# Kernel tuning notes

Hardware: AMD Instinct MI355X
Metric: run time of the kernel (lower is better)

The kernel has to match this reference:

```python
import jax, jax.numpy as jnp
import numpy as np

T, B, C, HS, RD = 32, 32, 128, 512, 3  # timesteps, batch, state_channels, hidden_size, recurse_depth
HW = 7


def setup_inputs() -> dict:
    key = jax.random.key(0)
    ks = jax.random.split(key, 6)
    x = jax.random.normal(ks[0], (T * B, C, HW, HW), jnp.float32)
    hxs = jax.random.normal(ks[1], (B, 2 * C, HW, HW), jnp.float32)
    masks = jax.random.uniform(ks[2], (T * B,), jnp.float32)
    # ConvLSTMCell: conv over concat(x, h) [2C in] -> 4C gate channels, 3x3, bias
    Wconv = jax.random.normal(ks[3], (4 * C, 2 * C, 3, 3), jnp.float32) * 0.02
    bconv = jnp.zeros((4 * C,), jnp.float32)
    # flat_lin: Linear(C*7*7 -> hidden_size), torch layout [out, in]
    Wlin = jax.random.normal(ks[4], (HS, C * HW * HW), jnp.float32) * 0.02
    blin = jnp.zeros((HS,), jnp.float32)
    return {"x": x, "hxs": hxs, "masks": masks, "Wconv": Wconv, "bconv": bconv, "Wlin": Wlin, "blin": blin}


def reference(x, hxs, masks, Wconv, bconv, Wlin, blin):
    xs = x.reshape(T, B, C, HW, HW)
    ms = masks.reshape(T, B)
    h0, c0 = hxs[:, :C], hxs[:, C:]

    def conv_gates(inp):  # [B, 2C, 7, 7] -> [B, 4C, 7, 7]
        y = jax.lax.conv_general_dilated(
            inp, Wconv, window_strides=(1, 1), padding="SAME",
            dimension_numbers=("NCHW", "OIHW", "NCHW"))
        return y + bconv[None, :, None, None]

    def step(carry, inp):
        h, c = carry
        x_t, m_t = inp
        m = m_t[:, None, None, None]
        h = h * m
        c = c * m
        for _ in range(RD):  # recurse_depth inner unroll (sequential dependency)
            g = conv_gates(jnp.concatenate([x_t, h], axis=1))
            cc_i, cc_f, cc_o, cc_g = jnp.split(g, 4, axis=1)
            i = jax.nn.sigmoid(cc_i)
            f = jax.nn.sigmoid(cc_f)
            o = jax.nn.sigmoid(cc_o)
            gg = jnp.tanh(cc_g)
            c = f * c + i * gg
            h = o * jnp.tanh(c)
        out = jax.nn.relu(c.reshape(B, -1) @ Wlin.T + blin)  # flat_lin applied to c
        return (h, c), out

    (hT, cT), outs = jax.lax.scan(step, (h0, c0), (xs, ms))
    return outs.reshape(T * B, HS), jnp.concatenate([hT, cT], axis=1)
```

## Files before the change

kernel.cpp:

```cpp
#include <hip/hip_runtime.h>
#include <hip/hip_bf16.h>
#include <stdint.h>

#define T_  32
#define B_  32
#define C_  128
#define HS_ 512
#define HW_ 7
#define S_  49
#define CS_  (C_*S_)
#define ICS_ (2*C_*S_)
#define KH_  1152
#define KL_  6272
#define M_   1568
#define MR_  1600
#define N_   512

typedef __attribute__((ext_vector_type(8))) short short8;
typedef __attribute__((ext_vector_type(4))) float f32x4;
typedef __hip_bfloat16 bf16;

union bfbits { bf16 b; short s; };

__device__ __forceinline__ void gl16(const void* g, void* l) {
    __builtin_amdgcn_global_load_lds((const __attribute__((address_space(1))) void*)g,
                                     (__attribute__((address_space(3))) void*)l, 16, 0, 0);
}

__device__ __forceinline__ float sigm_f(float v) { return 1.0f / (1.0f + __expf(-v)); }
__device__ __forceinline__ float tanh_f(float v) { return 1.0f - 2.0f / (__expf(2.0f * v) + 1.0f); }

__global__ __launch_bounds__(256, 2) void k_fgemm(
    const bf16* __restrict__ xTt, const bf16* __restrict__ hT,
    bf16* __restrict__ hTN,
    const bf16* __restrict__ WxP, const bf16* __restrict__ WhP,
    const float* __restrict__ bconv,
    float* __restrict__ Gx, float* __restrict__ cbuf,
    const float* __restrict__ mask_c, const float* __restrict__ mask_a,
    bf16* __restrict__ chist_t, const bf16* __restrict__ zb, int mode0)
{
    __shared__ __align__(16) uint8_t smem[65536];
    bf16* sA = (bf16*)smem;
    bf16* sB = (bf16*)(smem + 32768);
    float (*gld)[68] = (float(*)[68])smem;

    const int tid = threadIdx.x, lane = tid & 63, w = tid >> 6;
    const int wr = w >> 1, wc = w & 1;
    const int m0 = blockIdx.x * 64, n0 = blockIdx.y * 64;

    const int kq = tid & 15, rr = tid >> 4;
    const int swz = ((kq ^ rr) << 3);
    int abS[4], ay[4], ax[4]; bool rok[4];
#pragma unroll
    for (int q = 0; q < 4; ++q) {
        int ra = m0 + q * 16 + rr;
        rok[q] = ra < M_;
        int b = ra / S_, s = ra - b * S_;
        abS[q] = b * S_;
        ay[q] = s / HW_; ax[q] = s - ay[q] * HW_;
    }

    const int NS = mode0 ? 18 : 9;

    f32x4 accX[2][2], accH[2][2];
    if (mode0) {
#pragma unroll
        for (int fn = 0; fn < 2; ++fn) {
            int np = n0 + wc * 32 + fn * 16 + (lane & 15);
            float bv = bconv[((np & 3) << 7) + (np >> 2)];
            f32x4 b4 = {bv, bv, bv, bv};
            accX[0][fn] = b4; accX[1][fn] = b4;
            f32x4 z4 = {0.f, 0.f, 0.f, 0.f};
            accH[0][fn] = z4; accH[1][fn] = z4;
        }
    } else {
#pragma unroll
        for (int fm = 0; fm < 2; ++fm) {
            int row = m0 + wr * 32 + fm * 16 + ((lane >> 4) << 2);
#pragma unroll
            for (int fn = 0; fn < 2; ++fn) {
                int col = n0 + wc * 32 + fn * 16 + (lane & 15);
#pragma unroll
                for (int j = 0; j < 4; ++j)
                    accH[fm][fn][j] = Gx[(size_t)(row + j) * N_ + col];
            }
        }
    }

    auto stage = [&](int st, int dbuf) {
        int xph = (mode0 && st < 9);
        int kid = xph ? st : (mode0 ? st - 9 : st);
        int ky = kid / 3, kx = kid - ky * 3;
        const bf16* Asrc = xph ? xTt : hT;
        const bf16* Wsrc = xph ? WxP : WhP;
        bf16* lA = sA + dbuf * 8192;
        bf16* lB = sB + dbuf * 8192;
#pragma unroll
        for (int q = 0; q < 4; ++q) {
            int y2 = ay[q] + ky - 1, x2 = ax[q] + kx - 1;
            const bf16* rb = (rok[q] && (unsigned)y2 < (unsigned)HW_ && (unsigned)x2 < (unsigned)HW_)
                ? Asrc + (((size_t)(abS[q] + y2 * HW_ + x2)) << 7) : zb;
            gl16(rb + swz, lA + q * 2048 + w * 512);
            gl16(Wsrc + (size_t)(n0 + q * 16 + rr) * KH_ + kid * 128 + swz, lB + q * 2048 + w * 512);
        }
    };

    auto compute = [&](int dbuf, f32x4 (&acc)[2][2]) {
        const bf16* lA = sA + dbuf * 8192;
        const bf16* lB = sB + dbuf * 8192;
        short8 af[2][4], bq[2][4];
#pragma unroll
        for (int kh = 0; kh < 4; ++kh) {
            int c = kh * 4 + (lane >> 4);
            int xr = (c ^ (lane & 15)) << 3;
#pragma unroll
            for (int fm = 0; fm < 2; ++fm) {
                int r = wr * 32 + fm * 16 + (lane & 15);
                af[fm][kh] = *(const short8*)(lA + r * 128 + xr);
            }
#pragma unroll
            for (int fn = 0; fn < 2; ++fn) {
                int r = wc * 32 + fn * 16 + (lane & 15);
                bq[fn][kh] = *(const short8*)(lB + r * 128 + xr);
            }
        }
#pragma unroll
        for (int kh = 0; kh < 4; ++kh)
#pragma unroll
            for (int fm = 0; fm < 2; ++fm)
#pragma unroll
                for (int fn = 0; fn < 2; ++fn)
                    acc[fm][fn] = __builtin_amdgcn_mfma_f32_16x16x32_bf16(
                        af[fm][kh], bq[fn][kh], acc[fm][fn], 0, 0, 0);
    };

    stage(0, 0);
    __syncthreads();
#pragma unroll 1
    for (int st = 0; st < NS; ++st) {
        if (st + 1 < NS) stage(st + 1, (st + 1) & 1);
        if (mode0 && st < 9) compute(st & 1, accX);
        else                 compute(st & 1, accH);
        __syncthreads();
    }

    if (mode0) {
#pragma unroll
        for (int fm = 0; fm < 2; ++fm) {
            int row = m0 + wr * 32 + fm * 16 + ((lane >> 4) << 2);
#pragma unroll
            for (int fn = 0; fn < 2; ++fn) {
                int col = n0 + wc * 32 + fn * 16 + (lane & 15);
#pragma unroll
                for (int j = 0; j < 4; ++j) {
                    Gx[(size_t)(row + j) * N_ + col] = accX[fm][fn][j];
                    accH[fm][fn][j] += accX[fm][fn][j];
                }
            }
        }
    }

#pragma unroll
    for (int fm = 0; fm < 2; ++fm)
#pragma unroll
        for (int fn = 0; fn < 2; ++fn) {
            int row = wr * 32 + fm * 16 + ((lane >> 4) << 2);
            int col = wc * 32 + fn * 16 + (lane & 15);
#pragma unroll
            for (int j = 0; j < 4; ++j) gld[row + j][col] = accH[fm][fn][j];
        }
    __syncthreads();

#pragma unroll
    for (int q2 = 0; q2 < 4; ++q2) {
        int e = tid + q2 * 256;
        int row = e >> 4, cc = e & 15;
        int m = m0 + row;
        if (m >= M_) continue;
        int b = m / S_, s = m - b * S_;
        int cg = (n0 >> 2) + cc;
        float g0 = gld[row][cc * 4 + 0], g1 = gld[row][cc * 4 + 1];
        float g2 = gld[row][cc * 4 + 2], g3 = gld[row][cc * 4 + 3];
        float ig = sigm_f(g0);
        float fg = sigm_f(g1);
        float og = sigm_f(g2);
        float gg = tanh_f(g3);
        size_t ci = (((size_t)b * S_ + s) << 7) + cg;
        float co = cbuf[ci];
        if (mask_c) co *= mask_c[b];
        float cn = fg * co + ig * gg;
        cbuf[ci] = cn;
        float hn = og * tanh_f(cn);
        float am = mask_a ? mask_a[b] : 1.f;
        hTN[ci] = __float2bfloat16(hn * am);
        if (chist_t) chist_t[(size_t)b * KL_ + s * C_ + cg] = __float2bfloat16(cn);
    }
}

__global__ __launch_bounds__(256, 2) void k_lingemm(
    const bf16* __restrict__ Ac, const bf16* __restrict__ Wl,
    const float* __restrict__ blin, float* __restrict__ out)
{
    __shared__ __align__(16) uint8_t smem[65536];
    bf16* sA = (bf16*)smem;
    bf16* sB = (bf16*)(smem + 32768);

    const int tid = threadIdx.x, lane = tid & 63, w = tid >> 6;
    const int wr = w >> 1, wc = w & 1;
    const int m0 = blockIdx.x * 64, n0 = blockIdx.y * 64;
    const int kq = tid & 15, rr = tid >> 4;
    const int swz = ((kq ^ rr) << 3);

    f32x4 acc[2][2];
#pragma unroll
    for (int fn = 0; fn < 2; ++fn) {
        int np = n0 + wc * 32 + fn * 16 + (lane & 15);
        float bv = blin[np];
        f32x4 b4 = {bv, bv, bv, bv};
        acc[0][fn] = b4; acc[1][fn] = b4;
    }

    auto stage = [&](int st, int dbuf) {
        bf16* lA = sA + dbuf * 8192;
        bf16* lB = sB + dbuf * 8192;
#pragma unroll
        for (int q = 0; q < 4; ++q) {
            gl16(Ac + (size_t)(m0 + q * 16 + rr) * KL_ + st * 128 + swz, lA + q * 2048 + w * 512);
            gl16(Wl + (size_t)(n0 + q * 16 + rr) * KL_ + st * 128 + swz, lB + q * 2048 + w * 512);
        }
    };
    auto compute = [&](int dbuf) {
        const bf16* lA = sA + dbuf * 8192;
        const bf16* lB = sB + dbuf * 8192;
        short8 af[2][4], bq[2][4];
#pragma unroll
        for (int kh = 0; kh < 4; ++kh) {
            int c = kh * 4 + (lane >> 4);
            int xr = (c ^ (lane & 15)) << 3;
#pragma unroll
            for (int fm = 0; fm < 2; ++fm) {
                int r = wr * 32 + fm * 16 + (lane & 15);
                af[fm][kh] = *(const short8*)(lA + r * 128 + xr);
            }
#pragma unroll
            for (int fn = 0; fn < 2; ++fn) {
                int r = wc * 32 + fn * 16 + (lane & 15);
                bq[fn][kh] = *(const short8*)(lB + r * 128 + xr);
            }
        }
#pragma unroll
        for (int kh = 0; kh < 4; ++kh)
#pragma unroll
            for (int fm = 0; fm < 2; ++fm)
#pragma unroll
                for (int fn = 0; fn < 2; ++fn)
                    acc[fm][fn] = __builtin_amdgcn_mfma_f32_16x16x32_bf16(
                        af[fm][kh], bq[fn][kh], acc[fm][fn], 0, 0, 0);
    };

    stage(0, 0);
    __syncthreads();
#pragma unroll 1
    for (int st = 0; st < 49; ++st) {
        if (st + 1 < 49) stage(st + 1, (st + 1) & 1);
        compute(st & 1);
        __syncthreads();
    }

#pragma unroll
    for (int fm = 0; fm < 2; ++fm)
#pragma unroll
        for (int fn = 0; fn < 2; ++fn) {
            int col = n0 + wc * 32 + fn * 16 + (lane & 15);
            int rb  = m0 + wr * 32 + fm * 16 + ((lane >> 4) << 2);
#pragma unroll
            for (int j = 0; j < 4; ++j)
                out[(size_t)(rb + j) * N_ + col] = fmaxf(acc[fm][fn][j], 0.f);
        }
}

__global__ __launch_bounds__(256) void k_wsplit(const float* __restrict__ Wc,
                                               bf16* __restrict__ WxP, bf16* __restrict__ WhP) {
    int idx = blockIdx.x * 256 + threadIdx.x;
    if (idx >= 512 * 288) return;
    int np = idx / 288, kq = idx % 288;
    int oc = ((np & 3) << 7) + (np >> 2);
    int kk = kq * 8;
    int half = kk >= KH_;
    int krel = kk - half * KH_;
    short8 v;
#pragma unroll
    for (int j = 0; j < 8; ++j) {
        int kr = krel + j;
        int kid = kr >> 7, ic = (kr & 127) + half * 128;
        bfbits bb; bb.b = __float2bfloat16(Wc[((size_t)oc * 256 + ic) * 9 + kid]);
        v[j] = bb.s;
    }
    bf16* dst = half ? WhP : WxP;
    *reinterpret_cast<short8*>(dst + (size_t)np * KH_ + krel) = v;
}

__global__ __launch_bounds__(256) void k_wlin2(const float* __restrict__ Wl, bf16* __restrict__ Wp) {
    int idx = blockIdx.x * 256 + threadIdx.x;
    if (idx >= 512 * 784) return;
    int np = idx / 784, kq = idx % 784;
    short8 v;
#pragma unroll
    for (int j = 0; j < 8; ++j) {
        int kp = kq * 8 + j;
        int s = kp >> 7, c = kp & 127;
        bfbits bb; bb.b = __float2bfloat16(Wl[(size_t)np * KL_ + c * S_ + s]);
        v[j] = bb.s;
    }
    *reinterpret_cast<short8*>(Wp + (size_t)np * KL_ + kq * 8) = v;
}

__global__ __launch_bounds__(256) void k_xpose(const float* __restrict__ x, bf16* __restrict__ xT) {
    int idx = blockIdx.x * 256 + threadIdx.x;
    if (idx >= 1024 * 784) return;
    int r = idx / 784;
    int rem = idx % 784;
    int s = rem / 16, c8 = (rem & 15) * 8;
    const float* sp = x + (size_t)r * CS_ + c8 * S_ + s;
    short8 v;
#pragma unroll
    for (int j = 0; j < 8; ++j) { bfbits bb; bb.b = __float2bfloat16(sp[j * S_]); v[j] = bb.s; }
    *reinterpret_cast<short8*>(xT + (((size_t)r * S_ + s) << 7) + c8) = v;
}

__global__ __launch_bounds__(256) void k_hcprep(const float* __restrict__ hxs,
                                                const float* __restrict__ mask0,
                                                bf16* __restrict__ hT, float* __restrict__ cbuf) {
    int idx = blockIdx.x * 256 + threadIdx.x;
    if (idx >= 32 * 784) return;
    int b = idx / 784;
    int rem = idx % 784;
    int s = rem / 16, c8 = (rem & 15) * 8;
    float m = mask0[b];
    const float* hp = hxs + (size_t)b * ICS_ + c8 * S_ + s;
    const float* cp = hp + CS_;
    size_t o = (((size_t)b * S_ + s) << 7) + c8;
    short8 v;
#pragma unroll
    for (int j = 0; j < 8; ++j) {
        bfbits bb; bb.b = __float2bfloat16(hp[j * S_] * m); v[j] = bb.s;
        cbuf[o + j] = cp[j * S_];
    }
    *reinterpret_cast<short8*>(hT + o) = v;
}

__global__ __launch_bounds__(256) void k_zero16(uint4* __restrict__ p, int n) {
    int i = blockIdx.x * 256 + threadIdx.x;
    if (i < n) p[i] = make_uint4(0, 0, 0, 0);
}

__global__ __launch_bounds__(256) void k_final(const bf16* __restrict__ hT, const float* __restrict__ cbuf,
                                               float* __restrict__ out) {
    int i = blockIdx.x * 256 + threadIdx.x;
    if (i >= B_ * ICS_) return;
    int b = i / ICS_, r = i % ICS_;
    int ch = r / S_, s = r % S_;
    size_t o = (((size_t)b * S_ + s) << 7);
    out[i] = (ch < C_) ? __bfloat162float(hT[o + ch]) : cbuf[o + (ch - C_)];
}

extern "C" void kernel_launch(void* const* d_in, const int* in_sizes, int n_in,
                              void* d_out, int out_size, void* d_ws, size_t ws_size,
                              hipStream_t stream) {
    (void)in_sizes; (void)n_in; (void)out_size; (void)ws_size;
    const float* x     = (const float*)d_in[0];
    const float* hxs   = (const float*)d_in[1];
    const float* masks = (const float*)d_in[2];
    const float* Wconv = (const float*)d_in[3];
    const float* bconv = (const float*)d_in[4];
    const float* Wlin  = (const float*)d_in[5];
    const float* blin  = (const float*)d_in[6];
    float* out = (float*)d_out;

    uint8_t* p = (uint8_t*)d_ws;
    bf16* WxP   = (bf16*)p;   p += (size_t)512 * KH_ * 2;
    bf16* WhP   = (bf16*)p;   p += (size_t)512 * KH_ * 2;
    bf16* Wlp   = (bf16*)p;   p += (size_t)512 * KL_ * 2;
    bf16* xT    = (bf16*)p;   p += (size_t)1024 * S_ * C_ * 2;
    bf16* hA    = (bf16*)p;   p += (size_t)B_ * S_ * C_ * 2;
    bf16* hB    = (bf16*)p;   p += (size_t)B_ * S_ * C_ * 2;
    float* cbuf = (float*)p;  p += (size_t)B_ * S_ * C_ * 4;
    float* Gx   = (float*)p;  p += (size_t)MR_ * N_ * 4;
    bf16* chist = (bf16*)p;   p += (size_t)1024 * KL_ * 2;
    bf16* zb    = (bf16*)p;   p += 1024;
    bf16* hbufs[2] = {hA, hB};

    k_wsplit<<<576, 256, 0, stream>>>(Wconv, WxP, WhP);
    k_wlin2<<<1568, 256, 0, stream>>>(Wlin, Wlp);
    k_xpose<<<3136, 256, 0, stream>>>(x, xT);
    k_hcprep<<<98, 256, 0, stream>>>(hxs, masks, hA, cbuf);
    k_zero16<<<1, 256, 0, stream>>>((uint4*)zb, 64);

    int g = 0;
    for (int t = 0; t < T_; ++t) {
        const bf16* xTt = xT + (size_t)t * B_ * S_ * C_;
        for (int rd = 0; rd < 3; ++rd) {
            const float* mc = (rd == 0) ? masks + (size_t)t * B_ : nullptr;
            const float* ma = (rd == 2 && t < T_ - 1) ? masks + (size_t)(t + 1) * B_ : nullptr;
            bf16* ct = (rd == 2) ? chist + (size_t)t * B_ * KL_ : nullptr;
            k_fgemm<<<dim3(25, 8), 256, 0, stream>>>(
                (rd == 0) ? xTt : nullptr, hbufs[g & 1], hbufs[(g + 1) & 1],
                WxP, WhP, bconv, Gx, cbuf, mc, ma, ct, zb, (rd == 0) ? 1 : 0);
            ++g;
        }
    }

    k_lingemm<<<dim3(16, 8), 256, 0, stream>>>(chist, Wlp, blin, out);
    k_final<<<1568, 256, 0, stream>>>(hbufs[0], cbuf, out + (size_t)T_ * B_ * HS_);
}
```

Before: 1.403 ms.

## Switch GEMM kernels to triple-buffered LDS pipeline with counted vmcnt waits

Both the conv-gate GEMM and the linear GEMM move from double to triple LDS buffering. Each iteration prefetches two stages ahead and waits only until the older stage's global-to-LDS loads have landed (vmcnt(8)) rather than fully draining, so more memory latency overlaps with MFMA work. LDS grows to 96KB and launch bounds drop to one block per SM, which cuts occupancy. Correctness relies on the vmcnt count matching the number of loads issued per stage.

```diff
diff --git a/kernel.cpp b/kernel.cpp
--- a/kernel.cpp
+++ b/kernel.cpp
@@ -30,7 +30,20 @@
 __device__ __forceinline__ float sigm_f(float v) { return 1.0f / (1.0f + __expf(-v)); }
 __device__ __forceinline__ float tanh_f(float v) { return 1.0f - 2.0f / (__expf(2.0f * v) + 1.0f); }
 
-__global__ __launch_bounds__(256, 2) void k_fgemm(
+#define PIPE_BARRIER_COUNTED()  do {                                   \
+    asm volatile("s_waitcnt vmcnt(8)" ::: "memory");                   \
+    __builtin_amdgcn_sched_barrier(0);                                 \
+    __builtin_amdgcn_s_barrier();                                      \
+    __builtin_amdgcn_sched_barrier(0);                                 \
+} while (0)
+#define PIPE_BARRIER_DRAIN()  do {                                     \
+    asm volatile("s_waitcnt vmcnt(0)" ::: "memory");                   \
+    __builtin_amdgcn_sched_barrier(0);                                 \
+    __builtin_amdgcn_s_barrier();                                      \
+    __builtin_amdgcn_sched_barrier(0);                                 \
+} while (0)
+
+__global__ __launch_bounds__(256, 1) void k_fgemm(
     const bf16* __restrict__ xTt, const bf16* __restrict__ hT,
     bf16* __restrict__ hTN,
     const bf16* __restrict__ WxP, const bf16* __restrict__ WhP,
@@ -39,9 +52,9 @@
     const float* __restrict__ mask_c, const float* __restrict__ mask_a,
     bf16* __restrict__ chist_t, const bf16* __restrict__ zb, int mode0)
 {
-    __shared__ __align__(16) uint8_t smem[65536];
+    __shared__ __align__(16) uint8_t smem[98304];
     bf16* sA = (bf16*)smem;
-    bf16* sB = (bf16*)(smem + 32768);
+    bf16* sB = (bf16*)(smem + 49152);
     float (*gld)[68] = (float(*)[68])smem;
 
     const int tid = threadIdx.x, lane = tid & 63, w = tid >> 6;
@@ -135,14 +148,21 @@
     };
 
     stage(0, 0);
-    __syncthreads();
+    stage(1, 1);
+    PIPE_BARRIER_COUNTED();
+
+    int cur = 0;
 #pragma unroll 1
     for (int st = 0; st < NS; ++st) {
-        if (st + 1 < NS) stage(st + 1, (st + 1) & 1);
-        if (mode0 && st < 9) compute(st & 1, accX);
-        else                 compute(st & 1, accH);
-        __syncthreads();
-    }
+        int pre = cur + 2; if (pre >= 3) pre -= 3;
+        if (st + 2 < NS) stage(st + 2, pre);
+        if (mode0 && st < 9) compute(cur, accX);
+        else                 compute(cur, accH);
+        if (st + 2 < NS) { PIPE_BARRIER_COUNTED(); }
+        else             { PIPE_BARRIER_DRAIN(); }
+        ++cur; if (cur == 3) cur = 0;
+    }
+    __syncthreads();
 
     if (mode0) {
 #pragma unroll
@@ -197,13 +217,13 @@
     }
 }
 
-__global__ __launch_bounds__(256, 2) void k_lingemm(
+__global__ __launch_bounds__(256, 1) void k_lingemm(
     const bf16* __restrict__ Ac, const bf16* __restrict__ Wl,
     const float* __restrict__ blin, float* __restrict__ out)
 {
-    __shared__ __align__(16) uint8_t smem[65536];
+    __shared__ __align__(16) uint8_t smem[98304];
     bf16* sA = (bf16*)smem;
-    bf16* sB = (bf16*)(smem + 32768);
+    bf16* sB = (bf16*)(smem + 49152);
 
     const int tid = threadIdx.x, lane = tid & 63, w = tid >> 6;
     const int wr = w >> 1, wc = w & 1;
@@ -259,12 +279,18 @@
     };
 
     stage(0, 0);
-    __syncthreads();
+    stage(1, 1);
+    PIPE_BARRIER_COUNTED();
+
+    int cur = 0;
 #pragma unroll 1
     for (int st = 0; st < 49; ++st) {
-        if (st + 1 < 49) stage(st + 1, (st + 1) & 1);
-        compute(st & 1);
-        __syncthreads();
+        int pre = cur + 2; if (pre >= 3) pre -= 3;
+        if (st + 2 < 49) stage(st + 2, pre);
+        compute(cur);
+        if (st + 2 < 49) { PIPE_BARRIER_COUNTED(); }
+        else             { PIPE_BARRIER_DRAIN(); }
+        ++cur; if (cur == 3) cur = 0;
     }
 
 #pragma unroll
```

New measurement: 1.464 ms. 1.04x slower.
